# Optimization experiments

Measured on AMD Instinct MI355X. Metric: run time of the kernel, lower is better.

The kernel has to match this reference:

```python
import jax, jax.numpy as jnp
import numpy as np

D_MODEL, SEQ, D_HEAD, N_HEAD, D_MLP = 1024, 2048, 64, 16, 4096
BATCH = 2
LN_EPS = 1e-5


def layer_norm(x, gamma, beta):
    mu = jnp.mean(x, axis=-1, keepdims=True)
    var = jnp.mean(jnp.square(x - mu), axis=-1, keepdims=True)
    return (x - mu) * jax.lax.rsqrt(var + LN_EPS) * gamma + beta


def setup_inputs() -> dict:
    key = jax.random.key(0)
    ks = jax.random.split(key, 10)
    s = 1.0 / np.sqrt(D_MODEL)
    x = jax.random.normal(ks[0], (BATCH, SEQ, D_MODEL), dtype=jnp.float32)
    # per-head Q/K/V projections, stacked: [H, d_model, d_head]
    wq = jax.random.uniform(ks[1], (N_HEAD, D_MODEL, D_HEAD), jnp.float32, -s, s)
    wk = jax.random.uniform(ks[2], (N_HEAD, D_MODEL, D_HEAD), jnp.float32, -s, s)
    wv = jax.random.uniform(ks[3], (N_HEAD, D_MODEL, D_HEAD), jnp.float32, -s, s)
    wo = jax.random.uniform(ks[4], (N_HEAD * D_HEAD, D_MODEL), jnp.float32, -s, s)
    sm = 1.0 / np.sqrt(D_MLP)
    w_in = jax.random.uniform(ks[5], (D_MODEL, D_MLP), jnp.float32, -s, s)
    b_in = jax.random.uniform(ks[6], (D_MLP,), jnp.float32, -s, s)
    w_out = jax.random.uniform(ks[7], (D_MLP, D_MODEL), jnp.float32, -sm, sm)
    b_out = jax.random.uniform(ks[8], (D_MODEL,), jnp.float32, -sm, sm)
    g1 = jnp.ones((D_MODEL,), jnp.float32)
    bt1 = jnp.zeros((D_MODEL,), jnp.float32)
    g2 = jnp.ones((D_MODEL,), jnp.float32)
    bt2 = jnp.zeros((D_MODEL,), jnp.float32)
    return {"x": x, "wq": wq, "wk": wk, "wv": wv, "wo": wo,
            "w_in": w_in, "b_in": b_in, "w_out": w_out, "b_out": b_out,
            "g1": g1, "bt1": bt1, "g2": g2, "bt2": bt2}


def reference(x, wq, wk, wv, wo, w_in, b_in, w_out, b_out, g1, bt1, g2, bt2):
    B, S, D = x.shape
    # multi-head attention (all heads batched)
    q = jnp.einsum('bsd,hde->bhse', x, wq)  # [B,H,S,dh]
    k = jnp.einsum('bsd,hde->bhse', x, wk)
    v = jnp.einsum('bsd,hde->bhse', x, wv)
    scores = jnp.einsum('bhie,bhje->bhij', q, k) / np.sqrt(D_HEAD)
    causal = jnp.tril(jnp.ones((S, S), dtype=bool))
    scores = jnp.where(causal, scores, -jnp.inf)
    attn = jax.nn.softmax(scores, axis=-1)
    head_out = jnp.einsum('bhij,bhje->bhie', attn, v)  # [B,H,S,dh]
    # concat heads in order (head 0 first) -> [B,S,H*dh]
    head_out = jnp.transpose(head_out, (0, 2, 1, 3)).reshape(B, S, N_HEAD * D_HEAD)
    x = x + layer_norm(head_out @ wo, g1, bt1)
    mlp = jax.nn.relu(x @ w_in + b_in) @ w_out + b_out
    x = x + layer_norm(mlp, g2, bt2)
    return x
```

## Files before the change

### kernel.cpp

```cpp
#include <hip/hip_runtime.h>
#include <hip/hip_bf16.h>
#include <math.h>

#define DM 1024
#define SEQ 2048
#define DH 64
#define NH 16
#define DMLP 4096
#define BATCH 2
#define ROWS (BATCH*SEQ)

typedef __attribute__((ext_vector_type(4))) float f32x4;
typedef __attribute__((ext_vector_type(8))) short bf16x8;

__device__ __forceinline__ void gl2lds16(const __hip_bfloat16* g, __hip_bfloat16* l) {
  __builtin_amdgcn_global_load_lds(
      (const __attribute__((address_space(1))) void*)g,
      (__attribute__((address_space(3))) void*)l, 16, 0, 0);
}

template<int K, int OUT_BF16, int BIAS, int RELU>
__global__ __launch_bounds__(512) void gemm256(
    const __hip_bfloat16* __restrict__ A,
    const __hip_bfloat16* __restrict__ BT,
    float* __restrict__ Cf,
    __hip_bfloat16* __restrict__ Cb,
    const float* __restrict__ bias,
    int N)
{
  constexpr int NT = K / 64;
  __shared__ __align__(16) __hip_bfloat16 As[2][16384];
  __shared__ __align__(16) __hip_bfloat16 Bs[2][16384];
  const int t    = threadIdx.x;
  const int wave = t >> 6;
  const int lane = t & 63;
  const int col  = lane & 15;
  const int quad = lane >> 4;
  const int m0 = blockIdx.x * 256;
  const int n0 = blockIdx.y * 256;
  const int wm = (wave >> 2) * 128;
  const int wn = (wave & 3) * 64;

  const int tr = t >> 3;
  const int tc = (t & 7) ^ (tr & 7);
  const __hip_bfloat16* gA = A  + (size_t)(m0 + tr) * K + tc * 8;
  const __hip_bfloat16* gB = BT + (size_t)(n0 + tr) * K + tc * 8;

  const int sw  = col & 7;
  const int ao0 = ((quad)     ^ sw) * 8;
  const int ao1 = ((4 + quad) ^ sw) * 8;

  f32x4 acc[8][4] = {};

#define STAGE_A(h, u) do {                                                     \
    gl2lds16(gA + (size_t)(h)*128*K + (u)*64,                                  \
             &As[(u)&1][(h)*8192 + wave*512]);                                 \
    gl2lds16(gA + (size_t)(h)*128*K + (u)*64 + (size_t)64*K,                   \
             &As[(u)&1][(h)*8192 + 4096 + wave*512]);                          \
  } while (0)
#define STAGE_B(h, u) do {                                                     \
    gl2lds16(gB + (size_t)(h)*128*K + (u)*64,                                  \
             &Bs[(u)&1][(h)*8192 + wave*512]);                                 \
    gl2lds16(gB + (size_t)(h)*128*K + (u)*64 + (size_t)64*K,                   \
             &Bs[(u)&1][(h)*8192 + 4096 + wave*512]);                          \
  } while (0)
#define LOAD_A(base) do { _Pragma("unroll")                                    \
    for (int i = 0; i < 4; ++i) {                                              \
      af[i][0] = *(const bf16x8*)(pA + (base) + i*1024 + ao0);                 \
      af[i][1] = *(const bf16x8*)(pA + (base) + i*1024 + ao1);                 \
    } } while (0)
#define LOAD_BX(arr, base) do { _Pragma("unroll")                              \
    for (int j = 0; j < 2; ++j) {                                              \
      arr[j][0] = *(const bf16x8*)(pB + (base) + j*1024 + ao0);                \
      arr[j][1] = *(const bf16x8*)(pB + (base) + j*1024 + ao1);                \
    } } while (0)
#define PHASE_TAIL(MB, NB, BARR) do {                                          \
    asm volatile("s_barrier" ::: "memory");                                    \
    asm volatile("s_waitcnt lgkmcnt(0)" ::: "memory");                         \
    __builtin_amdgcn_s_setprio(1);                                             \
    _Pragma("unroll")                                                          \
    for (int kk = 0; kk < 2; ++kk)                                             \
      _Pragma("unroll")                                                        \
      for (int i = 0; i < 4; ++i)                                              \
        _Pragma("unroll")                                                      \
        for (int j = 0; j < 2; ++j)                                            \
          acc[(MB)+i][(NB)+j] = __builtin_amdgcn_mfma_f32_16x16x32_bf16(       \
              af[i][kk], BARR[j][kk], acc[(MB)+i][(NB)+j], 0, 0, 0);           \
    __builtin_amdgcn_s_setprio(0);                                             \
    asm volatile("s_barrier" ::: "memory");                                    \
  } while (0)

  STAGE_A(0, 0); STAGE_B(0, 0); STAGE_A(1, 0); STAGE_B(1, 0);
  if (NT > 1) {
    STAGE_A(0, 1); STAGE_B(0, 1); STAGE_A(1, 1); STAGE_B(1, 1);
    asm volatile("s_waitcnt vmcnt(8)" ::: "memory");
  } else {
    asm volatile("s_waitcnt vmcnt(0)" ::: "memory");
  }
  asm volatile("s_barrier" ::: "memory");

  #pragma unroll 2
  for (int u = 0; u < NT; ++u) {
    const __hip_bfloat16* pA = As[u & 1] + (wm + col) * 64;
    const __hip_bfloat16* pB = Bs[u & 1] + (wn + col) * 64;
    const bool s2 = (u + 2 < NT);
    bf16x8 af[4][2], bl[2][2], bh[2][2];

    LOAD_A(0);
    LOAD_BX(bl, 0);
    PHASE_TAIL(0, 0, bl);

    LOAD_BX(bh, 2048);
    PHASE_TAIL(0, 2, bh);

    LOAD_A(4096);
    if (s2) { STAGE_B(0, u + 2); STAGE_B(1, u + 2); }
    PHASE_TAIL(4, 2, bh);

    if (s2) {
      STAGE_A(0, u + 2); STAGE_A(1, u + 2);
      asm volatile("s_waitcnt vmcnt(8)" ::: "memory");
    } else {
      asm volatile("s_waitcnt vmcnt(0)" ::: "memory");
    }
    PHASE_TAIL(4, 0, bl);
  }
#undef STAGE_A
#undef STAGE_B
#undef LOAD_A
#undef LOAD_BX
#undef PHASE_TAIL

  #pragma unroll
  for (int mi = 0; mi < 8; ++mi) {
    #pragma unroll
    for (int ni = 0; ni < 4; ++ni) {
      const int cn = n0 + wn + ni*16 + col;
      float bv = 0.f;
      if (BIAS) bv = bias[cn];
      #pragma unroll
      for (int r = 0; r < 4; ++r) {
        const int cm = m0 + wm + mi*16 + quad*4 + r;
        float v = acc[mi][ni][r];
        if (BIAS) v += bv;
        if (RELU) v = fmaxf(v, 0.f);
        if (OUT_BF16) Cb[(size_t)cm * N + cn] = __float2bfloat16(v);
        else          Cf[(size_t)cm * N + cn] = v;
      }
    }
  }
}

template<int KS>
__global__ __launch_bounds__(512) void gemm256x128(
    const __hip_bfloat16* __restrict__ A,
    const __hip_bfloat16* __restrict__ BT,
    float* __restrict__ Cf,
    int N, int K, long long zstride)
{
  constexpr int NT = KS / 64;
  static_assert(NT >= 2, "pipeline needs >=2 K-tiles");
  __shared__ __align__(16) __hip_bfloat16 As[2][16384];
  __shared__ __align__(16) __hip_bfloat16 Bs[2][8192];
  const int t    = threadIdx.x;
  const int wave = t >> 6;
  const int lane = t & 63;
  const int col  = lane & 15;
  const int quad = lane >> 4;
  const int m0 = blockIdx.x * 256;
  const int n0 = blockIdx.y * 128;
  const int kz = (int)blockIdx.z * KS;
  const int wm = (wave >> 1) * 64;
  const int wn = (wave & 1) * 64;

  const int tr = t >> 3;
  const int tc = (t & 7) ^ (tr & 7);
  const __hip_bfloat16* gA = A  + (size_t)(m0 + tr) * K + kz + tc * 8;
  const __hip_bfloat16* gB = BT + (size_t)(n0 + tr) * K + kz + tc * 8;

  const int sw  = col & 7;
  const int ao0 = ((quad)     ^ sw) * 8;
  const int ao1 = ((4 + quad) ^ sw) * 8;

  f32x4 acc[4][4] = {};

#define SA(u) do { _Pragma("unroll")                                           \
    for (int q = 0; q < 4; ++q)                                                \
      gl2lds16(gA + (size_t)(q*64)*K + (u)*64,                                 \
               &As[(u)&1][q*4096 + wave*512]);                                 \
  } while (0)
#define SB(u) do { _Pragma("unroll")                                           \
    for (int q = 0; q < 2; ++q)                                                \
      gl2lds16(gB + (size_t)(q*64)*K + (u)*64,                                 \
               &Bs[(u)&1][q*4096 + wave*512]);                                 \
  } while (0)

  SA(0); SB(0); SA(1);

  #pragma unroll 2
  for (int v = 0; v < NT; ++v) {
    const __hip_bfloat16* pA = As[v & 1] + (wm + col) * 64;
    const __hip_bfloat16* pB = Bs[v & 1] + (wn + col) * 64;
    bf16x8 af[4][2], bf[4][2];

    if (v + 1 < NT) {
      SB(v + 1);
      asm volatile("s_waitcnt vmcnt(6)" ::: "memory");
    } else {
      asm volatile("s_waitcnt vmcnt(0)" ::: "memory");
    }
    asm volatile("s_barrier" ::: "memory");
    #pragma unroll
    for (int i = 0; i < 4; ++i) {
      af[i][0] = *(const bf16x8*)(pA + i*1024 + ao0);
      af[i][1] = *(const bf16x8*)(pA + i*1024 + ao1);
    }
    #pragma unroll
    for (int j = 0; j < 2; ++j) {
      bf[j][0] = *(const bf16x8*)(pB + j*1024 + ao0);
      bf[j][1] = *(const bf16x8*)(pB + j*1024 + ao1);
    }
    asm volatile("s_waitcnt lgkmcnt(0)" ::: "memory");
    __builtin_amdgcn_s_setprio(1);
    #pragma unroll
    for (int kk = 0; kk < 2; ++kk)
      #pragma unroll
      for (int i = 0; i < 4; ++i)
        #pragma unroll
        for (int j = 0; j < 2; ++j)
          acc[i][j] = __builtin_amdgcn_mfma_f32_16x16x32_bf16(
              af[i][kk], bf[j][kk], acc[i][j], 0, 0, 0);
    __builtin_amdgcn_s_setprio(0);
    asm volatile("s_barrier" ::: "memory");

    if (v + 2 < NT) SA(v + 2);
    #pragma unroll
    for (int j = 2; j < 4; ++j) {
      bf[j][0] = *(const bf16x8*)(pB + j*1024 + ao0);
      bf[j][1] = *(const bf16x8*)(pB + j*1024 + ao1);
    }
    asm volatile("s_waitcnt lgkmcnt(0)" ::: "memory");
    __builtin_amdgcn_s_setprio(1);
    #pragma unroll
    for (int kk = 0; kk < 2; ++kk)
      #pragma unroll
      for (int i = 0; i < 4; ++i)
        #pragma unroll
        for (int j = 2; j < 4; ++j)
          acc[i][j] = __builtin_amdgcn_mfma_f32_16x16x32_bf16(
              af[i][kk], bf[j][kk], acc[i][j], 0, 0, 0);
    __builtin_amdgcn_s_setprio(0);
    asm volatile("s_barrier" ::: "memory");
  }
#undef SA
#undef SB

  float* Co = Cf + (size_t)blockIdx.z * zstride;
  #pragma unroll
  for (int i = 0; i < 4; ++i) {
    #pragma unroll
    for (int j = 0; j < 4; ++j) {
      const int cn = n0 + wn + j*16 + col;
      #pragma unroll
      for (int r = 0; r < 4; ++r) {
        const int cm = m0 + wm + i*16 + quad*4 + r;
        Co[(size_t)cm * N + cn] = acc[i][j][r];
      }
    }
  }
}

__global__ __launch_bounds__(256) void attn_kernel(
    const __hip_bfloat16* __restrict__ qkv,
    const __hip_bfloat16* __restrict__ vt,
    __hip_bfloat16* __restrict__ aout)
{
  __shared__ __align__(16) __hip_bfloat16 Ks[2][64*64];
  __shared__ __align__(16) __hip_bfloat16 Vts[2][64*64];
  __shared__ __align__(16) __hip_bfloat16 Ps[4][16*64];

  const int bh = blockIdx.x, b = bh >> 4, h = bh & 15;
  const int t = threadIdx.x, wave = t >> 6, lane = t & 63;
  const int col = lane & 15, quad = lane >> 4;
  const float SC = 0.125f * 1.44269504f;

  const int r0  = t >> 3;
  const int cs0 = (t & 7) ^ (r0 & 7);
  const __hip_bfloat16* kbase = qkv + (size_t)b*SEQ*3072 + 1024 + h*64;
  const __hip_bfloat16* vbase = vt + (size_t)bh*64*SEQ;

#define AISSUE(j0, buf) do {                                                      \
    gl2lds16(kbase + (size_t)((j0) + r0)*3072      + cs0*8, &Ks[buf][wave*512]);  \
    gl2lds16(kbase + (size_t)((j0) + 32 + r0)*3072 + cs0*8, &Ks[buf][2048 + wave*512]); \
    gl2lds16(vbase + (size_t)r0*SEQ        + (j0) + cs0*8,  &Vts[buf][wave*512]); \
    gl2lds16(vbase + (size_t)(32 + r0)*SEQ + (j0) + cs0*8,  &Vts[buf][2048 + wave*512]); \
  } while (0)

  const int tile = 31 - (int)blockIdx.y;
  const int i0 = tile * 64;
  const int i0w = i0 + wave*16;

  bf16x8 aq[2];
  #pragma unroll
  for (int kk = 0; kk < 2; kk++)
    aq[kk] = *(const bf16x8*)&qkv[((size_t)(b*SEQ + i0w + col))*3072 + h*64 + kk*32 + quad*8];

  f32x4 O[4] = {};
  float lsum[4] = {0.f, 0.f, 0.f, 0.f};

  const int njt = tile + 1;
  AISSUE(0, 0);
  for (int jt = 0; jt < njt; jt++) {
    const int cur = jt & 1;
    const int j0 = jt * 64;
    __syncthreads();
    if (jt + 1 < njt) AISSUE(j0 + 64, cur ^ 1);

    f32x4 S[4] = {};
    __builtin_amdgcn_s_setprio(1);
    #pragma unroll
    for (int kk = 0; kk < 2; kk++) {
      const int sl = ((kk*4 + quad) ^ (col & 7)) * 8;
      #pragma unroll
      for (int jl = 0; jl < 4; jl++) {
        bf16x8 bk = *(const bf16x8*)&Ks[cur][(jl*16 + col)*64 + sl];
        S[jl] = __builtin_amdgcn_mfma_f32_16x16x32_bf16(aq[kk], bk, S[jl], 0, 0, 0);
      }
    }
    __builtin_amdgcn_s_setprio(0);

    const bool diag = (jt == tile);
    #pragma unroll
    for (int r = 0; r < 4; r++) {
      const int row = quad*4 + r;
      const int ig = i0 + wave*16 + row;
      #pragma unroll
      for (int jl = 0; jl < 4; jl++) {
        float p = exp2f(S[jl][r] * SC);
        if (diag && (j0 + jl*16 + col > ig)) p = 0.f;
        lsum[r] += p;
        const int c = jl*2 + (col >> 3);
        Ps[wave][row*64 + (c ^ (row & 7))*8 + (col & 7)] = __float2bfloat16(p);
      }
    }

    __builtin_amdgcn_s_setprio(1);
    #pragma unroll
    for (int kk = 0; kk < 2; kk++) {
      const int sl = ((kk*4 + quad) ^ (col & 7)) * 8;
      bf16x8 ap = *(const bf16x8*)&Ps[wave][col*64 + sl];
      #pragma unroll
      for (int et = 0; et < 4; et++) {
        bf16x8 bv = *(const bf16x8*)&Vts[cur][(et*16 + col)*64 + sl];
        O[et] = __builtin_amdgcn_mfma_f32_16x16x32_bf16(ap, bv, O[et], 0, 0, 0);
      }
    }
    __builtin_amdgcn_s_setprio(0);
  }

  #pragma unroll
  for (int r = 0; r < 4; r++) {
    float s = lsum[r];
    s += __shfl_xor(s, 1);
    s += __shfl_xor(s, 2);
    s += __shfl_xor(s, 4);
    s += __shfl_xor(s, 8);
    const float inv = 1.f / s;
    const int m = b*SEQ + i0w + quad*4 + r;
    #pragma unroll
    for (int et = 0; et < 4; et++)
      aout[(size_t)m*DM + h*64 + et*16 + col] = __float2bfloat16(O[et][r] * inv);
  }
#undef AISSUE
}

__global__ __launch_bounds__(256) void ln_res(
    const float* __restrict__ y0,
    const float* __restrict__ y1,
    const float* __restrict__ bias,
    const float* __restrict__ xres,
    float* __restrict__ xout,
    __hip_bfloat16* __restrict__ bout,
    const float* __restrict__ gamma,
    const float* __restrict__ beta)
{
  const int row = blockIdx.x;
  const int t = threadIdx.x;
  float4 v = ((const float4*)(y0 + (size_t)row*DM))[t];
  if (y1) {
    const float4 w = ((const float4*)(y1 + (size_t)row*DM))[t];
    v.x += w.x; v.y += w.y; v.z += w.z; v.w += w.w;
  }
  if (bias) {
    const float4 w = ((const float4*)bias)[t];
    v.x += w.x; v.y += w.y; v.z += w.z; v.w += w.w;
  }
  float s  = v.x + v.y + v.z + v.w;
  float sq = v.x*v.x + v.y*v.y + v.z*v.z + v.w*v.w;
  #pragma unroll
  for (int off = 32; off > 0; off >>= 1) {
    s  += __shfl_down(s, off);
    sq += __shfl_down(sq, off);
  }
  __shared__ float red[8];
  const int wave = t >> 6, lane = t & 63;
  if (lane == 0) { red[wave] = s; red[4 + wave] = sq; }
  __syncthreads();
  s  = red[0] + red[1] + red[2] + red[3];
  sq = red[4] + red[5] + red[6] + red[7];
  const float mu   = s * (1.f/DM);
  const float var  = sq * (1.f/DM) - mu*mu;
  const float rstd = rsqrtf(var + 1e-5f);
  const float4 g  = ((const float4*)gamma)[t];
  const float4 bt = ((const float4*)beta)[t];
  const float4 xr = ((const float4*)(xres + (size_t)row*DM))[t];
  float4 o;
  o.x = (v.x - mu)*rstd*g.x + bt.x + xr.x;
  o.y = (v.y - mu)*rstd*g.y + bt.y + xr.y;
  o.z = (v.z - mu)*rstd*g.z + bt.z + xr.z;
  o.w = (v.w - mu)*rstd*g.w + bt.w + xr.w;
  ((float4*)(xout + (size_t)row*DM))[t] = o;
  if (bout) {
    __hip_bfloat16* bp = bout + (size_t)row*DM + t*4;
    bp[0] = __float2bfloat16(o.x);
    bp[1] = __float2bfloat16(o.y);
    bp[2] = __float2bfloat16(o.z);
    bp[3] = __float2bfloat16(o.w);
  }
}

__global__ __launch_bounds__(256) void transpose_cvt(
    const float* __restrict__ src, __hip_bfloat16* __restrict__ dst,
    int K, int N, long long sz, long long dz)
{
  __shared__ float tile[32][33];
  const int z = blockIdx.z;
  const int k0 = blockIdx.y * 32, n0 = blockIdx.x * 32;
  const int tx = threadIdx.x & 31, ty = threadIdx.x >> 5;
  const float* s = src + (size_t)z*sz;
  __hip_bfloat16* d = dst + (size_t)z*dz;
  for (int i = ty; i < 32; i += 8)
    tile[i][tx] = s[(size_t)(k0+i)*N + n0 + tx];
  __syncthreads();
  for (int i = ty; i < 32; i += 8)
    d[(size_t)(n0+i)*K + k0 + tx] = __float2bfloat16(tile[tx][i]);
}

__global__ __launch_bounds__(256) void transpose_v(
    const __hip_bfloat16* __restrict__ qkv, __hip_bfloat16* __restrict__ vt)
{
  __shared__ __hip_bfloat16 tile[32][33];
  const int bh = blockIdx.z, b = bh >> 4, h = bh & 15;
  const int s0 = blockIdx.x * 32, e0 = blockIdx.y * 32;
  const int tx = threadIdx.x & 31, ty = threadIdx.x >> 5;
  for (int i = ty; i < 32; i += 8)
    tile[i][tx] = qkv[(size_t)(b*SEQ + s0+i)*3072 + 2048 + h*64 + e0 + tx];
  __syncthreads();
  for (int i = ty; i < 32; i += 8)
    vt[((size_t)bh*64 + e0+i)*SEQ + s0 + tx] = tile[tx][i];
}

__global__ __launch_bounds__(256) void cvt_bf16(
    const float* __restrict__ src, __hip_bfloat16* __restrict__ dst, int n4)
{
  const int i = blockIdx.x*256 + threadIdx.x;
  if (i < n4) {
    const float4 v = ((const float4*)src)[i];
    dst[i*4+0] = __float2bfloat16(v.x);
    dst[i*4+1] = __float2bfloat16(v.y);
    dst[i*4+2] = __float2bfloat16(v.z);
    dst[i*4+3] = __float2bfloat16(v.w);
  }
}

extern "C" void kernel_launch(void* const* d_in, const int* in_sizes, int n_in,
                              void* d_out, int out_size, void* d_ws, size_t ws_size,
                              hipStream_t stream)
{
  const float* x     = (const float*)d_in[0];
  const float* wq    = (const float*)d_in[1];
  const float* wk    = (const float*)d_in[2];
  const float* wv    = (const float*)d_in[3];
  const float* wo    = (const float*)d_in[4];
  const float* w_in  = (const float*)d_in[5];
  const float* b_in  = (const float*)d_in[6];
  const float* w_out = (const float*)d_in[7];
  const float* b_out = (const float*)d_in[8];
  const float* g1    = (const float*)d_in[9];
  const float* bt1   = (const float*)d_in[10];
  const float* g2    = (const float*)d_in[11];
  const float* bt2   = (const float*)d_in[12];
  float* out = (float*)d_out;

  char* ws = (char*)d_ws;
  __hip_bfloat16* xb     = (__hip_bfloat16*)(ws + 0);
  __hip_bfloat16* wqkvT  = (__hip_bfloat16*)(ws + 8388608);
  __hip_bfloat16* woT    = (__hip_bfloat16*)(ws + 14680064);
  __hip_bfloat16* w_inT  = (__hip_bfloat16*)(ws + 16777216);
  __hip_bfloat16* w_outT = (__hip_bfloat16*)(ws + 25165824);
  __hip_bfloat16* qkvb   = (__hip_bfloat16*)(ws + 33554432);
  __hip_bfloat16* vtb    = (__hip_bfloat16*)(ws + 58720256);
  __hip_bfloat16* attn_o = (__hip_bfloat16*)(ws + 67108864);
  float*          P0     = (float*)(ws + 33554432);
  float*          x1     = (float*)(ws + 75497472);
  __hip_bfloat16* x1b    = (__hip_bfloat16*)(ws + 92274688);
  __hip_bfloat16* hbuf   = (__hip_bfloat16*)(ws + 33554432);
  float*          M0     = (float*)(ws + 0);
  float*          M1     = (float*)(ws + 100663296);
  float*          P1     = (float*)(ws + 50331648);

  const long long PROJ_ZS = (long long)ROWS * DM;
  const long long MLP_ZS  = 100663296LL / 4;

  cvt_bf16<<<ROWS*DM/4/256, 256, 0, stream>>>(x, xb, ROWS*DM/4);

  transpose_cvt<<<dim3(2,32,16), 256, 0, stream>>>(wq, wqkvT,             DM, DH, (long long)DM*DH, (long long)DH*DM);
  transpose_cvt<<<dim3(2,32,16), 256, 0, stream>>>(wk, wqkvT + 1024*1024, DM, DH, (long long)DM*DH, (long long)DH*DM);
  transpose_cvt<<<dim3(2,32,16), 256, 0, stream>>>(wv, wqkvT + 2048*1024, DM, DH, (long long)DM*DH, (long long)DH*DM);
  transpose_cvt<<<dim3(32,32,1),  256, 0, stream>>>(wo,    woT,    DM,   DM,   0, 0);
  transpose_cvt<<<dim3(128,32,1), 256, 0, stream>>>(w_in,  w_inT,  DM,   DMLP, 0, 0);
  transpose_cvt<<<dim3(32,128,1), 256, 0, stream>>>(w_out, w_outT, DMLP, DM,   0, 0);

  gemm256<DM,1,0,0><<<dim3(ROWS/256, 3072/256), 512, 0, stream>>>(xb, wqkvT, nullptr, qkvb, nullptr, 3072);
  transpose_v<<<dim3(SEQ/32, 2, BATCH*NH), 256, 0, stream>>>(qkvb, vtb);
  attn_kernel<<<dim3(BATCH*NH, SEQ/64), 256, 0, stream>>>(qkvb, vtb, attn_o);
  gemm256x128<512><<<dim3(ROWS/256, DM/128, 2), 512, 0, stream>>>(attn_o, woT, P0, DM, DM, PROJ_ZS);
  ln_res<<<ROWS, 256, 0, stream>>>(P0, P1, nullptr, x, x1, x1b, g1, bt1);
  gemm256<DM,1,1,1><<<dim3(ROWS/256, DMLP/256), 512, 0, stream>>>(x1b, w_inT, nullptr, hbuf, b_in, DMLP);
  gemm256x128<2048><<<dim3(ROWS/256, DM/128, 2), 512, 0, stream>>>(hbuf, w_outT, M0, DM, DMLP, MLP_ZS);
  ln_res<<<ROWS, 256, 0, stream>>>(M0, M1, b_out, x1, out, nullptr, g2, bt2);
}
```

Baseline: 234.6 us.

## Single-buffer V in attention with split waitcnts and serpentine tile order

The attention kernel now keeps K double-buffered but V in a single LDS buffer. V for the current tile is issued right after a raw s_barrier, and explicit vmcnt waits let the QK^T MFMAs start before V has arrived, overlapping the V load with score computation and softmax. This cuts LDS use, which may raise occupancy. The query-tile order also changes from heaviest-first to a serpentine order within groups of eight tiles, which may hurt load balance for the causal workload. The vmcnt waits are per wave and there is no barrier after them, so reading LDS rows loaded by other waves risks a race.

```diff
diff --git a/kernel.cpp b/kernel.cpp
--- a/kernel.cpp
+++ b/kernel.cpp
@@ -276,7 +276,7 @@
     __hip_bfloat16* __restrict__ aout)
 {
   __shared__ __align__(16) __hip_bfloat16 Ks[2][64*64];
-  __shared__ __align__(16) __hip_bfloat16 Vts[2][64*64];
+  __shared__ __align__(16) __hip_bfloat16 Vts[64*64];
   __shared__ __align__(16) __hip_bfloat16 Ps[4][16*64];
 
   const int bh = blockIdx.x, b = bh >> 4, h = bh & 15;
@@ -289,14 +289,17 @@
   const __hip_bfloat16* kbase = qkv + (size_t)b*SEQ*3072 + 1024 + h*64;
   const __hip_bfloat16* vbase = vt + (size_t)bh*64*SEQ;
 
-#define AISSUE(j0, buf) do {                                                      \
+#define KISSUE(j0, buf) do {                                                      \
     gl2lds16(kbase + (size_t)((j0) + r0)*3072      + cs0*8, &Ks[buf][wave*512]);  \
     gl2lds16(kbase + (size_t)((j0) + 32 + r0)*3072 + cs0*8, &Ks[buf][2048 + wave*512]); \
-    gl2lds16(vbase + (size_t)r0*SEQ        + (j0) + cs0*8,  &Vts[buf][wave*512]); \
-    gl2lds16(vbase + (size_t)(32 + r0)*SEQ + (j0) + cs0*8,  &Vts[buf][2048 + wave*512]); \
-  } while (0)
-
-  const int tile = 31 - (int)blockIdx.y;
+  } while (0)
+#define VISSUE(j0) do {                                                           \
+    gl2lds16(vbase + (size_t)r0*SEQ        + (j0) + cs0*8,  &Vts[wave*512]);      \
+    gl2lds16(vbase + (size_t)(32 + r0)*SEQ + (j0) + cs0*8,  &Vts[2048 + wave*512]); \
+  } while (0)
+
+  const int yq = (int)blockIdx.y >> 3, yr = (int)blockIdx.y & 7;
+  const int tile = (yq << 3) | ((yq & 1) ? (7 - yr) : yr);
   const int i0 = tile * 64;
   const int i0w = i0 + wave*16;
 
@@ -309,12 +312,19 @@
   float lsum[4] = {0.f, 0.f, 0.f, 0.f};
 
   const int njt = tile + 1;
-  AISSUE(0, 0);
+  KISSUE(0, 0);
   for (int jt = 0; jt < njt; jt++) {
     const int cur = jt & 1;
     const int j0 = jt * 64;
-    __syncthreads();
-    if (jt + 1 < njt) AISSUE(j0 + 64, cur ^ 1);
+    const bool pf = (jt + 1 < njt);
+    asm volatile("s_barrier" ::: "memory");
+    VISSUE(j0);
+    if (pf) {
+      KISSUE(j0 + 64, cur ^ 1);
+      asm volatile("s_waitcnt vmcnt(4)" ::: "memory");
+    } else {
+      asm volatile("s_waitcnt vmcnt(2)" ::: "memory");
+    }
 
     f32x4 S[4] = {};
     __builtin_amdgcn_s_setprio(1);
@@ -344,6 +354,9 @@
       }
     }
 
+    if (pf) asm volatile("s_waitcnt vmcnt(2)" ::: "memory");
+    else    asm volatile("s_waitcnt vmcnt(0)" ::: "memory");
+
     __builtin_amdgcn_s_setprio(1);
     #pragma unroll
     for (int kk = 0; kk < 2; kk++) {
@@ -351,7 +364,7 @@
       bf16x8 ap = *(const bf16x8*)&Ps[wave][col*64 + sl];
       #pragma unroll
       for (int et = 0; et < 4; et++) {
-        bf16x8 bv = *(const bf16x8*)&Vts[cur][(et*16 + col)*64 + sl];
+        bf16x8 bv = *(const bf16x8*)&Vts[(et*16 + col)*64 + sl];
         O[et] = __builtin_amdgcn_mfma_f32_16x16x32_bf16(ap, bv, O[et], 0, 0, 0);
       }
     }
@@ -371,7 +384,8 @@
     for (int et = 0; et < 4; et++)
       aout[(size_t)m*DM + h*64 + et*16 + col] = __float2bfloat16(O[et][r] * inv);
   }
-#undef AISSUE
+#undef KISSUE
+#undef VISSUE
 }
 
 __global__ __launch_bounds__(256) void ln_res(
```

Result: no change. 233.4 us (-0.5%).
